# Kernel tuning notes

Measured on AMD Instinct MI355X. Metric: run time of the kernel, lower is better.

Reference implementation:

```python
import jax, jax.numpy as jnp
from jax import lax
import numpy as np

T = 8192          # timesteps (segments)
TOTAL = 1048576   # total ally rows across all timesteps
D_SELF = 128
D_ALLY = 64
H = 20            # h_size_1 == h_size_2
NOUT = 16
LOG_STD_BOUND = 2.0  # Params().log_std_bound (class not shown in source)


def setup_inputs() -> dict:
    key = jax.random.key(0)
    ks = jax.random.split(key, 16)

    def w(k, shape, fan_in):
        b = 1.0 / np.sqrt(fan_in)
        return jax.random.uniform(k, shape, jnp.float32, -b, b)

    # sorted segment ids, every segment in [0,T) guaranteed nonempty
    seg = jnp.sort(jnp.concatenate([
        jnp.arange(T, dtype=jnp.int32),
        jax.random.randint(ks[0], (TOTAL - T,), 0, T, dtype=jnp.int32)]))

    return dict(
        self_input=jax.random.normal(ks[1], (T, D_SELF), jnp.float32),
        ally_input=jax.random.normal(ks[2], (TOTAL, D_ALLY), jnp.float32),
        segment_ids=seg,
        W_self=w(ks[3], (H, D_SELF), D_SELF), b_self=jnp.zeros(H, jnp.float32),
        W_ally=w(ks[4], (H, D_ALLY), D_ALLY), b_ally=jnp.zeros(H, jnp.float32),
        W_cat=w(ks[5], (H, 2 * H), 2 * H), b_cat=jnp.zeros(H, jnp.float32),
        W_ih=w(ks[6], (4 * H, H), H), W_hh=w(ks[7], (4 * H, H), H),
        b_ih=jnp.zeros(4 * H, jnp.float32), b_hh=jnp.zeros(4 * H, jnp.float32),
        W_pfc=w(ks[8], (H, H), H), b_pfc=jnp.zeros(H, jnp.float32),
        W_vfc=w(ks[9], (H, H), H), b_vfc=jnp.zeros(H, jnp.float32),
        W_mu=w(ks[10], (NOUT, H), H), b_mu=jnp.zeros(NOUT, jnp.float32),
        W_ls=w(ks[11], (NOUT, H), H), b_ls=jnp.zeros(NOUT, jnp.float32),
        W_v=w(ks[12], (1, H), H), b_v=jnp.zeros(1, jnp.float32),
        h0=jnp.zeros(H, jnp.float32), c0=jnp.zeros(H, jnp.float32),
    )


def reference(self_input, ally_input, segment_ids, W_self, b_self, W_ally, b_ally,
              W_cat, b_cat, W_ih, W_hh, b_ih, b_hh, W_pfc, b_pfc, W_vfc, b_vfc,
              W_mu, b_mu, W_ls, b_ls, W_v, b_v, h0, c0):
    # per-item Linear+tanh, then ragged mean per timestep (segment mean)
    s = jnp.tanh(self_input @ W_self.T + b_self)                 # [T,H]
    a = jnp.tanh(ally_input @ W_ally.T + b_ally)                 # [TOTAL,H]
    sums = jax.ops.segment_sum(a, segment_ids, num_segments=T)   # [T,H]
    cnts = jax.ops.segment_sum(jnp.ones((a.shape[0], 1), a.dtype),
                               segment_ids, num_segments=T)      # [T,1]
    avg = sums / cnts                                            # [T,H]

    cat_out = jnp.tanh(jnp.concatenate([s, avg], axis=1) @ W_cat.T + b_cat)  # [T,H]

    # single-layer LSTM over T steps (batch=1), torch gate order i,f,g,o
    xg = cat_out @ W_ih.T + (b_ih + b_hh)                        # [T,4H]

    def step(carry, g_x):
        h, c = carry
        g = g_x + W_hh @ h
        i = jax.nn.sigmoid(g[:H])
        f = jax.nn.sigmoid(g[H:2 * H])
        gg = jnp.tanh(g[2 * H:3 * H])
        o = jax.nn.sigmoid(g[3 * H:])
        c = f * c + i * gg
        h = o * jnp.tanh(c)
        return (h, c), h

    _, lstm_out = lax.scan(step, (h0, c0), xg)                   # [T,H]

    x = jnp.tanh(lstm_out @ W_pfc.T + b_pfc)
    mu = jnp.tanh(x @ W_mu.T + b_mu)                             # [T,NOUT]
    log_std = x @ W_ls.T + b_ls                                  # [T,NOUT]
    log_std_out = jnp.exp(jax.nn.relu(log_std) - LOG_STD_BOUND)

    xv = jnp.tanh(cat_out @ W_vfc.T + b_vfc)
    v = xv @ W_v.T + b_v                                         # [T,1]
    return mu, log_std_out, v, log_std
```

## Files before the change

### kernel.cpp

```cpp
#include <hip/hip_runtime.h>
#include <hip/hip_bf16.h>


#define T_STEPS 8192
#define TOTAL_ROWS 1048576
#define DSELF 128
#define DALLY 64
#define HS 20
#define NOUT 16
#define L2E 1.44269504088896340736f

typedef float v2f __attribute__((ext_vector_type(2)));

__device__ __forceinline__ float rcp_f(float x) { return __builtin_amdgcn_rcpf(x); }
__device__ __forceinline__ float sigm_f(float x) { return rcp_f(1.0f + __expf(-x)); }
__device__ __forceinline__ float tanh_f(float x) { return fmaf(2.0f, sigm_f(2.0f * x), -1.0f); }
__device__ __forceinline__ float sig2_f(float x) {
  return rcp_f(1.0f + __builtin_amdgcn_exp2f(-x));
}

__device__ __forceinline__ v2f pk_fma(v2f acc, v2f w, v2f h) {
  asm("v_pk_fma_f32 %0, %1, %2, %0" : "+v"(acc) : "v"(w), "s"(h));
  return acc;
}
__device__ __forceinline__ v2f pk_add(v2f a, v2f b) {
  v2f d;
  asm("v_pk_add_f32 %0, %1, %2" : "=v"(d) : "v"(a), "v"(b));
  return d;
}

__global__ void k_bounds(const int* __restrict__ seg, int* __restrict__ start) {
  int s = blockIdx.x * blockDim.x + threadIdx.x;
  if (s > T_STEPS) return;
  if (s == T_STEPS) { start[s] = TOTAL_ROWS; return; }
  int lo = 0, hi = TOTAL_ROWS;
  while (lo < hi) {
    int mid = (lo + hi) >> 1;
    if (seg[mid] < s) lo = mid + 1; else hi = mid;
  }
  start[s] = lo;
}

__global__ __launch_bounds__(64) void k_segmean(
    const float* __restrict__ ally, const int* __restrict__ start,
    const float* __restrict__ W_ally, const float* __restrict__ b_ally,
    float* __restrict__ avg) {
  __shared__ float tile[64][DALLY + 2];
  __shared__ float red[64][HS + 1];
  const int lane = threadIdx.x;
  const int s = blockIdx.x;
  const int r0 = start[s], r1 = start[s + 1];
  float acc[HS];
#pragma unroll
  for (int h = 0; h < HS; ++h) acc[h] = 0.0f;
  for (int base = r0; base < r1; base += 64) {
    const int m = min(64, r1 - base);
    __syncthreads();
    for (int idx = lane; idx < m * 16; idx += 64) {
      const int rr = idx >> 4, cc = (idx & 15) << 2;
      const float4 v = *reinterpret_cast<const float4*>(
          ally + (size_t)(base + rr) * DALLY + cc);
      *reinterpret_cast<float2*>(&tile[rr][cc])     = make_float2(v.x, v.y);
      *reinterpret_cast<float2*>(&tile[rr][cc + 2]) = make_float2(v.z, v.w);
    }
    __syncthreads();
    if (lane < m) {
      float dot[HS];
#pragma unroll
      for (int h = 0; h < HS; ++h) dot[h] = b_ally[h];
#pragma unroll
      for (int j = 0; j < DALLY; j += 4) {
        const float2 xa = *reinterpret_cast<const float2*>(&tile[lane][j]);
        const float2 xb = *reinterpret_cast<const float2*>(&tile[lane][j + 2]);
#pragma unroll
        for (int h = 0; h < HS; ++h) {
          const float4 w = *reinterpret_cast<const float4*>(&W_ally[h * DALLY + j]);
          dot[h] = fmaf(xa.x, w.x, dot[h]);
          dot[h] = fmaf(xa.y, w.y, dot[h]);
          dot[h] = fmaf(xb.x, w.z, dot[h]);
          dot[h] = fmaf(xb.y, w.w, dot[h]);
        }
      }
#pragma unroll
      for (int h = 0; h < HS; ++h) acc[h] += tanh_f(dot[h]);
    }
  }
#pragma unroll
  for (int h = 0; h < HS; ++h) red[lane][h] = acc[h];
  __syncthreads();
  if (lane < HS) {
    float t = 0.0f;
    for (int l = 0; l < 64; ++l) t += red[l][lane];
    avg[(size_t)s * HS + lane] = t / (float)(r1 - r0);
  }
}

__global__ __launch_bounds__(256) void k_feats(
    const float* __restrict__ self_in, const float* __restrict__ avg,
    const float* __restrict__ W_self, const float* __restrict__ b_self,
    const float* __restrict__ W_cat, const float* __restrict__ b_cat,
    const float* __restrict__ W_ih, const float* __restrict__ b_ih,
    const float* __restrict__ b_hh,
    const float* __restrict__ W_vfc, const float* __restrict__ b_vfc,
    const float* __restrict__ W_v, const float* __restrict__ b_v,
    float* __restrict__ xg, float* __restrict__ v_out) {
  __shared__ float s_ws[HS * DSELF];
  __shared__ float s_bs[HS];
  __shared__ float s_wc[HS * 2 * HS];
  __shared__ float s_bc[HS];
  __shared__ float s_wih[4 * HS * HS];
  __shared__ float s_bih[4 * HS];
  __shared__ float s_wv[HS * HS];
  __shared__ float s_bv[HS];
  __shared__ float s_wvv[HS];
  __shared__ float s_bvs;
  const int tid = threadIdx.x;
  for (int i = tid; i < HS * DSELF; i += 256) s_ws[i] = W_self[i];
  for (int i = tid; i < HS * 2 * HS; i += 256) s_wc[i] = W_cat[i];
  for (int i = tid; i < 4 * HS * HS; i += 256) {
    const float sc = (i >= 800 && i < 1200) ? (2.0f * L2E) : L2E;
    s_wih[i] = W_ih[i] * sc;
  }
  for (int i = tid; i < HS * HS; i += 256) s_wv[i] = W_vfc[i];
  if (tid < HS) {
    s_bs[tid] = b_self[tid]; s_bc[tid] = b_cat[tid];
    s_bv[tid] = b_vfc[tid];  s_wvv[tid] = W_v[tid];
  }
  if (tid < 4 * HS) {
    const float sc = (tid >= 40 && tid < 60) ? (2.0f * L2E) : L2E;
    s_bih[tid] = (b_ih[tid] + b_hh[tid]) * sc;
  }
  if (tid == 0) s_bvs = b_v[0];
  __syncthreads();

  const int t = blockIdx.x * 256 + tid;
  const float* srow = self_in + (size_t)t * DSELF;
  float acc[HS];
#pragma unroll
  for (int h = 0; h < HS; ++h) acc[h] = s_bs[h];
  for (int j = 0; j < DSELF / 4; ++j) {
    const float4 x = *reinterpret_cast<const float4*>(srow + j * 4);
#pragma unroll
    for (int h = 0; h < HS; ++h) {
      const float4 w = *reinterpret_cast<const float4*>(&s_ws[h * DSELF + j * 4]);
      acc[h] = fmaf(x.x, w.x, acc[h]);
      acc[h] = fmaf(x.y, w.y, acc[h]);
      acc[h] = fmaf(x.z, w.z, acc[h]);
      acc[h] = fmaf(x.w, w.w, acc[h]);
    }
  }
  float sv[HS], av[HS];
#pragma unroll
  for (int h = 0; h < HS; ++h) sv[h] = tanh_f(acc[h]);
  {
    const float4* ap = reinterpret_cast<const float4*>(avg + (size_t)t * HS);
#pragma unroll
    for (int q = 0; q < HS / 4; ++q) {
      const float4 a4 = ap[q];
      av[q * 4 + 0] = a4.x; av[q * 4 + 1] = a4.y;
      av[q * 4 + 2] = a4.z; av[q * 4 + 3] = a4.w;
    }
  }
  float cat[HS];
#pragma unroll
  for (int h = 0; h < HS; ++h) {
    float a = s_bc[h];
#pragma unroll
    for (int j = 0; j < HS; ++j) a = fmaf(sv[j], s_wc[h * 2 * HS + j], a);
#pragma unroll
    for (int j = 0; j < HS; ++j) a = fmaf(av[j], s_wc[h * 2 * HS + HS + j], a);
    cat[h] = tanh_f(a);
  }
#pragma unroll 2
  for (int jj = 0; jj < 4 * HS; jj += 4) {
    float a0 = s_bih[jj], a1 = s_bih[jj + 1], a2 = s_bih[jj + 2], a3 = s_bih[jj + 3];
#pragma unroll
    for (int k = 0; k < HS; ++k) {
      const float cv = cat[k];
      a0 = fmaf(cv, s_wih[(jj + 0) * HS + k], a0);
      a1 = fmaf(cv, s_wih[(jj + 1) * HS + k], a1);
      a2 = fmaf(cv, s_wih[(jj + 2) * HS + k], a2);
      a3 = fmaf(cv, s_wih[(jj + 3) * HS + k], a3);
    }
    float4 o4; o4.x = a0; o4.y = a1; o4.z = a2; o4.w = a3;
    *reinterpret_cast<float4*>(&xg[(size_t)t * 80 + jj]) = o4;
  }
  float vacc = s_bvs;
#pragma unroll
  for (int h = 0; h < HS; ++h) {
    float a = s_bv[h];
#pragma unroll
    for (int k = 0; k < HS; ++k) a = fmaf(cat[k], s_wv[h * HS + k], a);
    vacc = fmaf(tanh_f(a), s_wvv[h], vacc);
  }
  v_out[t] = vacc;
}

#define LSTM_STEP(X1, X2, K)                                                  \
  do {                                                                        \
    v2f pA = {(X1), 0.0f}, pB = {0.0f, 0.0f};                                 \
    v2f qA = {(X2), 0.0f}, qB = {0.0f, 0.0f};                                 \
    _Pragma("unroll") for (int j = 0; j < 10; j += 2) {                       \
      const v2f h2a = {hs[2 * j],     hs[2 * j + 1]};                         \
      const v2f h2b = {hs[2 * j + 2], hs[2 * j + 3]};                         \
      pA = pk_fma(pA, wa2[j],     h2a);                                       \
      qA = pk_fma(qA, wb2[j],     h2a);                                       \
      pB = pk_fma(pB, wa2[j + 1], h2b);                                       \
      qB = pk_fma(qB, wb2[j + 1], h2b);                                       \
    }                                                                         \
    pA = pk_add(pA, pB);                                                      \
    qA = pk_add(qA, qB);                                                      \
    const float a1 = pA.x + pA.y;                                             \
    const float a2 = qA.x + qA.y;                                             \
    (X1) = px1[(K + 8) * 80];                                                 \
    (X2) = px2[(K + 8) * 80];                                                 \
    const float t1 = sig2_f(a1);                                   \
    const float t2 = fmaf(Ac, sig2_f(a2), Bc);          \
    auto rfp = __builtin_amdgcn_permlane32_swap(                              \
        __float_as_uint(t1), __float_as_uint(t1), false, false);              \
    auto rop = __builtin_amdgcn_permlane32_swap(                              \
        __float_as_uint(t2), __float_as_uint(t2), false, false);              \
    const float fp = __uint_as_float(rfp[1]);                \
    const float op = __uint_as_float(rop[1]);                \
    cs = fmaf(fp, cs, t1 * t2);                              \
    const float op2 = op + op;                                  \
    const float u = sig2_f(cs);                                  \
    const float hn = fmaf(op2, u, -op);                      \
    if (lane < HS) hp[(K)*HS] = hn;                                           \
    const unsigned hu = __float_as_uint(hn);                                  \
    _Pragma("unroll") for (int j = 0; j < HS; ++j)                            \
        hs[j] = __uint_as_float(__builtin_amdgcn_readlane(hu, j));            \
  } while (0)

__global__ __launch_bounds__(64) void k_lstm(
    const float* __restrict__ xg, const float* __restrict__ Whh,
    const float* __restrict__ h0, const float* __restrict__ c0,
    float* __restrict__ hout) {
  const int lane = threadIdx.x;
  const int kk = lane & 31;
  const int kc = kk < HS ? kk : HS - 1;
  const int r1 = kc + ((lane >= 32) ? HS : 0);
  const int r2 = r1 + 2 * HS;

  const float Ac = (lane < 32) ? 4.0f * L2E : 1.0f;
  const float Bc = (lane < 32) ? -2.0f * L2E : 0.0f;
  const float s2v = (lane < 32) ? 2.0f * L2E : L2E;

  v2f wa2[10], wb2[10];
  {
    const v2f* ra = reinterpret_cast<const v2f*>(Whh + (size_t)r1 * HS);
    const v2f* rb = reinterpret_cast<const v2f*>(Whh + (size_t)r2 * HS);
#pragma unroll
    for (int j = 0; j < 10; ++j) {
      v2f a = ra[j], b = rb[j];
      a.x *= L2E; a.y *= L2E;
      b.x *= s2v; b.y *= s2v;
      wa2[j] = a; wb2[j] = b;
    }
  }

  float hs[HS];
#pragma unroll
  for (int j = 0; j < HS; ++j) hs[j] = h0[j];
  float cs = c0[kc] * (2.0f * L2E);

  const float* px1 = xg + r1;
  const float* px2 = xg + r2;
  float x10 = px1[0 * 80], x20 = px2[0 * 80];
  float x11 = px1[1 * 80], x21 = px2[1 * 80];
  float x12 = px1[2 * 80], x22 = px2[2 * 80];
  float x13 = px1[3 * 80], x23 = px2[3 * 80];
  float x14 = px1[4 * 80], x24 = px2[4 * 80];
  float x15 = px1[5 * 80], x25 = px2[5 * 80];
  float x16 = px1[6 * 80], x26 = px2[6 * 80];
  float x17 = px1[7 * 80], x27 = px2[7 * 80];
  float* hp = hout + lane;

  for (int t = 0; t < T_STEPS; t += 8) {
    LSTM_STEP(x10, x20, 0);
    LSTM_STEP(x11, x21, 1);
    LSTM_STEP(x12, x22, 2);
    LSTM_STEP(x13, x23, 3);
    LSTM_STEP(x14, x24, 4);
    LSTM_STEP(x15, x25, 5);
    LSTM_STEP(x16, x26, 6);
    LSTM_STEP(x17, x27, 7);
    px1 += 8 * 80; px2 += 8 * 80; hp += 8 * HS;
  }
}

__global__ __launch_bounds__(256) void k_heads(
    const float* __restrict__ hbuf,
    const float* __restrict__ W_pfc, const float* __restrict__ b_pfc,
    const float* __restrict__ W_mu, const float* __restrict__ b_mu,
    const float* __restrict__ W_ls, const float* __restrict__ b_ls,
    float* __restrict__ mu_out, float* __restrict__ lso_out,
    float* __restrict__ ls_out) {
  __shared__ float wp[HS * HS], bp[HS], wm[NOUT * HS], bm[NOUT], wl[NOUT * HS], bl[NOUT];
  const int tid = threadIdx.x;
  for (int i = tid; i < HS * HS; i += 256) wp[i] = W_pfc[i];
  for (int i = tid; i < NOUT * HS; i += 256) { wm[i] = W_mu[i]; wl[i] = W_ls[i]; }
  if (tid < HS) bp[tid] = b_pfc[tid];
  if (tid < NOUT) { bm[tid] = b_mu[tid]; bl[tid] = b_ls[tid]; }
  __syncthreads();
  const int t = blockIdx.x * 256 + tid;
  float hr[HS];
  {
    const float4* hp4 = reinterpret_cast<const float4*>(hbuf + (size_t)t * HS);
#pragma unroll
    for (int q = 0; q < HS / 4; ++q) {
      const float4 h4 = hp4[q];
      hr[q * 4 + 0] = h4.x; hr[q * 4 + 1] = h4.y;
      hr[q * 4 + 2] = h4.z; hr[q * 4 + 3] = h4.w;
    }
  }
  float x[HS];
#pragma unroll
  for (int h = 0; h < HS; ++h) {
    float a = bp[h];
#pragma unroll
    for (int k = 0; k < HS; ++k) a = fmaf(hr[k], wp[h * HS + k], a);
    x[h] = tanh_f(a);
  }
  float4* mo4 = reinterpret_cast<float4*>(mu_out + (size_t)t * NOUT);
  float4* lo4 = reinterpret_cast<float4*>(lso_out + (size_t)t * NOUT);
  float4* lb4 = reinterpret_cast<float4*>(ls_out + (size_t)t * NOUT);
#pragma unroll
  for (int m = 0; m < NOUT; m += 4) {
    float4 mu4, lsb4, lso4;
    float am[4], bm_[4];
#pragma unroll
    for (int q = 0; q < 4; ++q) { am[q] = bm[m + q]; bm_[q] = bl[m + q]; }
#pragma unroll
    for (int k = 0; k < HS; ++k) {
      const float xv = x[k];
#pragma unroll
      for (int q = 0; q < 4; ++q) {
        am[q]  = fmaf(xv, wm[(m + q) * HS + k], am[q]);
        bm_[q] = fmaf(xv, wl[(m + q) * HS + k], bm_[q]);
      }
    }
    mu4.x = tanh_f(am[0]); mu4.y = tanh_f(am[1]);
    mu4.z = tanh_f(am[2]); mu4.w = tanh_f(am[3]);
    lsb4.x = bm_[0]; lsb4.y = bm_[1]; lsb4.z = bm_[2]; lsb4.w = bm_[3];
    lso4.x = __expf(fmaxf(bm_[0], 0.0f) - 2.0f);
    lso4.y = __expf(fmaxf(bm_[1], 0.0f) - 2.0f);
    lso4.z = __expf(fmaxf(bm_[2], 0.0f) - 2.0f);
    lso4.w = __expf(fmaxf(bm_[3], 0.0f) - 2.0f);
    mo4[m / 4] = mu4; lb4[m / 4] = lsb4; lo4[m / 4] = lso4;
  }
}

extern "C" void kernel_launch(void* const* d_in, const int* in_sizes, int n_in,
                              void* d_out, int out_size, void* d_ws, size_t ws_size,
                              hipStream_t stream) {
  const float* self_in = (const float*)d_in[0];
  const float* ally_in = (const float*)d_in[1];
  const int*   seg     = (const int*)d_in[2];
  const float* W_self  = (const float*)d_in[3];
  const float* b_self  = (const float*)d_in[4];
  const float* W_ally  = (const float*)d_in[5];
  const float* b_ally  = (const float*)d_in[6];
  const float* W_cat   = (const float*)d_in[7];
  const float* b_cat   = (const float*)d_in[8];
  const float* W_ih    = (const float*)d_in[9];
  const float* W_hh    = (const float*)d_in[10];
  const float* b_ih    = (const float*)d_in[11];
  const float* b_hh    = (const float*)d_in[12];
  const float* W_pfc   = (const float*)d_in[13];
  const float* b_pfc   = (const float*)d_in[14];
  const float* W_vfc   = (const float*)d_in[15];
  const float* b_vfc   = (const float*)d_in[16];
  const float* W_mu    = (const float*)d_in[17];
  const float* b_mu    = (const float*)d_in[18];
  const float* W_ls    = (const float*)d_in[19];
  const float* b_ls    = (const float*)d_in[20];
  const float* W_v     = (const float*)d_in[21];
  const float* b_v     = (const float*)d_in[22];
  const float* h0      = (const float*)d_in[23];
  const float* c0      = (const float*)d_in[24];
  float* out = (float*)d_out;

  char* ws = (char*)d_ws;
  int*   start = (int*)(ws);
  float* avg   = (float*)(ws + 36864);
  float* xg    = (float*)(ws + 692224);
  float* hbuf  = (float*)(ws + 3313664);

  float* mu_out  = out;
  float* lso_out = out + 131072;
  float* v_out   = out + 262144;
  float* ls_out  = out + 270336;

  k_bounds<<<(T_STEPS + 256) / 256, 256, 0, stream>>>(seg, start);
  k_segmean<<<T_STEPS, 64, 0, stream>>>(ally_in, start, W_ally, b_ally, avg);
  k_feats<<<T_STEPS / 256, 256, 0, stream>>>(self_in, avg, W_self, b_self,
                                             W_cat, b_cat, W_ih, b_ih, b_hh,
                                             W_vfc, b_vfc, W_v, b_v, xg, v_out);
  k_lstm<<<1, 64, 0, stream>>>(xg, W_hh, h0, c0, hbuf);
  k_heads<<<T_STEPS / 256, 256, 0, stream>>>(hbuf, W_pfc, b_pfc, W_mu, b_mu,
                                             W_ls, b_ls, mu_out, lso_out, ls_out);
}
```

Baseline: 1.653 ms.

## Share one reciprocal across LSTM gates, fold bounds search into segmean, halve block sizes

The LSTM step now computes both gate sigmoids with a single reciprocal of the product of their denominators and pre-scales the output gate, which shortens the serial dependency chain in the recurrent loop. The separate k_bounds kernel is removed and each k_segmean block does its own binary search for its row range, saving one launch. k_feats and k_heads move from 256 to 128 threads per block for more blocks. Multiplying two denominators into one reciprocal risks overflow or precision loss when both exponentials are large.

```diff
diff --git a/kernel.cpp b/kernel.cpp
--- a/kernel.cpp
+++ b/kernel.cpp
@@ -15,9 +15,6 @@
 __device__ __forceinline__ float rcp_f(float x) { return __builtin_amdgcn_rcpf(x); }
 __device__ __forceinline__ float sigm_f(float x) { return rcp_f(1.0f + __expf(-x)); }
 __device__ __forceinline__ float tanh_f(float x) { return fmaf(2.0f, sigm_f(2.0f * x), -1.0f); }
-__device__ __forceinline__ float sig2_f(float x) {
-  return rcp_f(1.0f + __builtin_amdgcn_exp2f(-x));
-}
 
 __device__ __forceinline__ v2f pk_fma(v2f acc, v2f w, v2f h) {
   asm("v_pk_fma_f32 %0, %1, %2, %0" : "+v"(acc) : "v"(w), "s"(h));
@@ -29,27 +26,29 @@
   return d;
 }
 
-__global__ void k_bounds(const int* __restrict__ seg, int* __restrict__ start) {
-  int s = blockIdx.x * blockDim.x + threadIdx.x;
-  if (s > T_STEPS) return;
-  if (s == T_STEPS) { start[s] = TOTAL_ROWS; return; }
-  int lo = 0, hi = TOTAL_ROWS;
-  while (lo < hi) {
-    int mid = (lo + hi) >> 1;
-    if (seg[mid] < s) lo = mid + 1; else hi = mid;
-  }
-  start[s] = lo;
-}
-
 __global__ __launch_bounds__(64) void k_segmean(
-    const float* __restrict__ ally, const int* __restrict__ start,
+    const float* __restrict__ ally, const int* __restrict__ seg,
     const float* __restrict__ W_ally, const float* __restrict__ b_ally,
     float* __restrict__ avg) {
   __shared__ float tile[64][DALLY + 2];
   __shared__ float red[64][HS + 1];
   const int lane = threadIdx.x;
   const int s = blockIdx.x;
-  const int r0 = start[s], r1 = start[s + 1];
+  int r0;
+  {
+    int lo = 0, hi = TOTAL_ROWS;
+    while (lo < hi) { int mid = (lo + hi) >> 1; if (seg[mid] < s) lo = mid + 1; else hi = mid; }
+    r0 = lo;
+  }
+  int r1;
+  if (s == T_STEPS - 1) {
+    r1 = TOTAL_ROWS;
+  } else {
+    int lo = r0, hi = TOTAL_ROWS;
+    const int sp = s + 1;
+    while (lo < hi) { int mid = (lo + hi) >> 1; if (seg[mid] < sp) lo = mid + 1; else hi = mid; }
+    r1 = lo;
+  }
   float acc[HS];
 #pragma unroll
   for (int h = 0; h < HS; ++h) acc[h] = 0.0f;
@@ -95,7 +94,7 @@
   }
 }
 
-__global__ __launch_bounds__(256) void k_feats(
+__global__ __launch_bounds__(128) void k_feats(
     const float* __restrict__ self_in, const float* __restrict__ avg,
     const float* __restrict__ W_self, const float* __restrict__ b_self,
     const float* __restrict__ W_cat, const float* __restrict__ b_cat,
@@ -115,13 +114,13 @@
   __shared__ float s_wvv[HS];
   __shared__ float s_bvs;
   const int tid = threadIdx.x;
-  for (int i = tid; i < HS * DSELF; i += 256) s_ws[i] = W_self[i];
-  for (int i = tid; i < HS * 2 * HS; i += 256) s_wc[i] = W_cat[i];
-  for (int i = tid; i < 4 * HS * HS; i += 256) {
+  for (int i = tid; i < HS * DSELF; i += 128) s_ws[i] = W_self[i];
+  for (int i = tid; i < HS * 2 * HS; i += 128) s_wc[i] = W_cat[i];
+  for (int i = tid; i < 4 * HS * HS; i += 128) {
     const float sc = (i >= 800 && i < 1200) ? (2.0f * L2E) : L2E;
     s_wih[i] = W_ih[i] * sc;
   }
-  for (int i = tid; i < HS * HS; i += 256) s_wv[i] = W_vfc[i];
+  for (int i = tid; i < HS * HS; i += 128) s_wv[i] = W_vfc[i];
   if (tid < HS) {
     s_bs[tid] = b_self[tid]; s_bc[tid] = b_cat[tid];
     s_bv[tid] = b_vfc[tid];  s_wvv[tid] = W_v[tid];
@@ -133,7 +132,7 @@
   if (tid == 0) s_bvs = b_v[0];
   __syncthreads();
 
-  const int t = blockIdx.x * 256 + tid;
+  const int t = blockIdx.x * 128 + tid;
   const float* srow = self_in + (size_t)t * DSELF;
   float acc[HS];
 #pragma unroll
@@ -214,18 +213,26 @@
     const float a2 = qA.x + qA.y;                                             \
     (X1) = px1[(K + 8) * 80];                                                 \
     (X2) = px2[(K + 8) * 80];                                                 \
-    const float t1 = sig2_f(a1);                                   \
-    const float t2 = fmaf(Ac, sig2_f(a2), Bc);          \
+    const float e1 = __builtin_amdgcn_exp2f(-a1);                             \
+    const float e2 = __builtin_amdgcn_exp2f(-a2);                             \
+    const float d1 = 1.0f + e1;                                               \
+    const float d2 = 1.0f + e2;                                               \
+    const float R  = rcp_f(d1 * d2);                                          \
+    const float n  = fmaf(Bn, e2, An);               \
+    const float m  = fmaf(2.0f, e1, 2.0f);                   \
+    const float P1 = n * R;                                     \
+    const float P2 = m * R;                                    \
     auto rfp = __builtin_amdgcn_permlane32_swap(                              \
-        __float_as_uint(t1), __float_as_uint(t1), false, false);              \
+        __float_as_uint(P1), __float_as_uint(P1), false, false);              \
     auto rop = __builtin_amdgcn_permlane32_swap(                              \
-        __float_as_uint(t2), __float_as_uint(t2), false, false);              \
-    const float fp = __uint_as_float(rfp[1]);                \
-    const float op = __uint_as_float(rop[1]);                \
-    cs = fmaf(fp, cs, t1 * t2);                              \
-    const float op2 = op + op;                                  \
-    const float u = sig2_f(cs);                                  \
-    const float hn = fmaf(op2, u, -op);                      \
+        __float_as_uint(P2), __float_as_uint(P2), false, false);              \
+    const float fp  = __uint_as_float(rfp[1]);               \
+    const float op2 = __uint_as_float(rop[1]);             \
+    cs = fmaf(fp, cs, P1);                                   \
+    const float ho = -0.5f * op2;                               \
+    const float ec = __builtin_amdgcn_exp2f(-cs);                             \
+    const float uc = rcp_f(1.0f + ec);                           \
+    const float hn = fmaf(op2, uc, ho);                      \
     if (lane < HS) hp[(K)*HS] = hn;                                           \
     const unsigned hu = __float_as_uint(hn);                                  \
     _Pragma("unroll") for (int j = 0; j < HS; ++j)                            \
@@ -242,8 +249,8 @@
   const int r1 = kc + ((lane >= 32) ? HS : 0);
   const int r2 = r1 + 2 * HS;
 
-  const float Ac = (lane < 32) ? 4.0f * L2E : 1.0f;
-  const float Bc = (lane < 32) ? -2.0f * L2E : 0.0f;
+  const float An = (lane < 32) ? 2.0f * L2E : 1.0f;
+  const float Bn = (lane < 32) ? -2.0f * L2E : 1.0f;
   const float s2v = (lane < 32) ? 2.0f * L2E : L2E;
 
   v2f wa2[10], wb2[10];
@@ -289,7 +296,7 @@
   }
 }
 
-__global__ __launch_bounds__(256) void k_heads(
+__global__ __launch_bounds__(128) void k_heads(
     const float* __restrict__ hbuf,
     const float* __restrict__ W_pfc, const float* __restrict__ b_pfc,
     const float* __restrict__ W_mu, const float* __restrict__ b_mu,
@@ -298,12 +305,12 @@
     float* __restrict__ ls_out) {
   __shared__ float wp[HS * HS], bp[HS], wm[NOUT * HS], bm[NOUT], wl[NOUT * HS], bl[NOUT];
   const int tid = threadIdx.x;
-  for (int i = tid; i < HS * HS; i += 256) wp[i] = W_pfc[i];
-  for (int i = tid; i < NOUT * HS; i += 256) { wm[i] = W_mu[i]; wl[i] = W_ls[i]; }
+  for (int i = tid; i < HS * HS; i += 128) wp[i] = W_pfc[i];
+  for (int i = tid; i < NOUT * HS; i += 128) { wm[i] = W_mu[i]; wl[i] = W_ls[i]; }
   if (tid < HS) bp[tid] = b_pfc[tid];
   if (tid < NOUT) { bm[tid] = b_mu[tid]; bl[tid] = b_ls[tid]; }
   __syncthreads();
-  const int t = blockIdx.x * 256 + tid;
+  const int t = blockIdx.x * 128 + tid;
   float hr[HS];
   {
     const float4* hp4 = reinterpret_cast<const float4*>(hbuf + (size_t)t * HS);
@@ -382,7 +389,6 @@
   float* out = (float*)d_out;
 
   char* ws = (char*)d_ws;
-  int*   start = (int*)(ws);
   float* avg   = (float*)(ws + 36864);
   float* xg    = (float*)(ws + 692224);
   float* hbuf  = (float*)(ws + 3313664);
@@ -392,12 +398,11 @@
   float* v_out   = out + 262144;
   float* ls_out  = out + 270336;
 
-  k_bounds<<<(T_STEPS + 256) / 256, 256, 0, stream>>>(seg, start);
-  k_segmean<<<T_STEPS, 64, 0, stream>>>(ally_in, start, W_ally, b_ally, avg);
-  k_feats<<<T_STEPS / 256, 256, 0, stream>>>(self_in, avg, W_self, b_self,
+  k_segmean<<<T_STEPS, 64, 0, stream>>>(ally_in, seg, W_ally, b_ally, avg);
+  k_feats<<<T_STEPS / 128, 128, 0, stream>>>(self_in, avg, W_self, b_self,
                                              W_cat, b_cat, W_ih, b_ih, b_hh,
                                              W_vfc, b_vfc, W_v, b_v, xg, v_out);
   k_lstm<<<1, 64, 0, stream>>>(xg, W_hh, h0, c0, hbuf);
-  k_heads<<<T_STEPS / 256, 256, 0, stream>>>(hbuf, W_pfc, b_pfc, W_mu, b_mu,
+  k_heads<<<T_STEPS / 128, 128, 0, stream>>>(hbuf, W_pfc, b_pfc, W_mu, b_mu,
                                              W_ls, b_ls, mu_out, lso_out, ls_out);
 }
```

Result: faster. 1.570 ms (-5.0%).
